# Kernel optimization log

Measured on AMD Instinct MI355X. Metric: run time of the kernel, lower is better.

Reference implementation:

```python
import jax, jax.numpy as jnp
import numpy as np

OBS, ACT, H = 64, 16, 64
T, B = 512, 4096


def _orth(key, shape):
    # orthogonal init like nn.init.orthogonal_ (gain 1 for predict; capture uses
    # gain sqrt(2) via init_ wrapper, but predict re-inits to plain orthogonal).
    a = jax.random.normal(key, shape, dtype=jnp.float32)
    q, r = jnp.linalg.qr(a if shape[0] >= shape[1] else a.T)
    q = q * jnp.sign(jnp.diag(r))
    return q if shape[0] >= shape[1] else q.T


def setup_inputs() -> dict:
    key = jax.random.key(0)
    ks = jax.random.split(key, 10)
    g2 = np.sqrt(2.0).astype(np.float32)
    inp = {
        "x": jax.random.normal(ks[0], (T, B, OBS), dtype=jnp.float32),
        "h": jax.random.normal(ks[1], (1, B, H), dtype=jnp.float32),
        "g": jax.random.uniform(ks[2], (T, B, 1), dtype=jnp.float32),
        "a": jax.random.normal(ks[3], (T, B, ACT), dtype=jnp.float32),
        # capture MLP: Linear(obs->H), tanh, Linear(H->H), tanh  (gain sqrt(2))
        "Wc1": g2 * _orth(ks[4], (OBS, H)),
        "bc1": jnp.zeros((H,), jnp.float32),
        "Wc2": g2 * _orth(ks[5], (H, H)),
        "bc2": jnp.zeros((H,), jnp.float32),
        # predict (Dynamics): Linear(H+ACT->H), tanh, Linear(H->H), tanh (gain 1)
        "Wp1": _orth(ks[6], (H + ACT, H)),
        "bp1": jnp.zeros((H,), jnp.float32),
        "Wp2": _orth(ks[7], (H, H)),
        "bp2": jnp.zeros((H,), jnp.float32),
    }
    return inp


def reference(x, h, g, a, Wc1, bc1, Wc2, bc2, Wp1, bp1, Wp2, bp2):
    # capture branch has no recurrent dependence -> compute for all t at once
    z1_all = jnp.tanh(jnp.tanh(x @ Wc1 + bc1) @ Wc2 + bc2)  # [T, B, H]

    def step(h_prev, inp):  # h_prev: [B, H]
        z1_t, g_t, a_t = inp
        ha = jnp.concatenate([h_prev, a_t], axis=-1)  # [B, H+ACT]
        z2 = jnp.tanh(jnp.tanh(ha @ Wp1 + bp1) @ Wp2 + bp2)
        h_new = (1.0 - g_t) * z1_t + g_t * z2
        return h_new, h_new

    h_final, outs = jax.lax.scan(step, h[0], (z1_all, g, a))
    capt = z1_all.reshape(-1, z1_all.shape[-1])  # torch.cat over [B,H] chunks -> [T*B, H]
    return outs, h_final[None], capt
```

## Files before the change

kernel.cpp:

```cpp
#include <hip/hip_runtime.h>
#include <hip/hip_bf16.h>

#define T_STEPS 512
#define BATCH   4096
#define ACT     16
#define HDIM    64
#define HA_S    168
#define T1_S    168
#define Z1_S    66

typedef short s8v __attribute__((ext_vector_type(8)));
typedef float f4v __attribute__((ext_vector_type(4)));

#define MFMA16(A, B, C) __builtin_amdgcn_mfma_f32_16x16x32_bf16((A), (B), (C), 0, 0, 0)

__device__ __forceinline__ unsigned pkbf(float a, float b) {
    unsigned r;
    asm("v_cvt_pk_bf16_f32 %0, %1, %2" : "=v"(r) : "v"(a), "v"(b));
    return r;
}
__device__ __forceinline__ float lo16f(unsigned p) { return __builtin_bit_cast(float, p << 16); }
__device__ __forceinline__ float hi16f(unsigned p) { return __builtin_bit_cast(float, p & 0xFFFF0000u); }

__device__ __forceinline__ unsigned short f2bf(float f) {
    unsigned u = __builtin_bit_cast(unsigned, f);
    u += 0x7FFFu + ((u >> 16) & 1u);
    return (unsigned short)(u >> 16);
}
__device__ __forceinline__ float bf2f(unsigned short b) {
    return __builtin_bit_cast(float, ((unsigned)b) << 16);
}

__device__ __forceinline__ float ftanh(float x) {
    float e = __expf(2.0f * x);
    return 1.0f - 2.0f * __builtin_amdgcn_rcpf(e + 1.0f);
}

#define BAR() do { \
    asm volatile("s_waitcnt lgkmcnt(0)" ::: "memory"); \
    __builtin_amdgcn_s_barrier(); \
    asm volatile("" ::: "memory"); \
} while (0)

__device__ __forceinline__ void stage_x(short* xsb, int row, int col, float4 v) {
    unsigned h0 = pkbf(v.x, v.y), h1 = pkbf(v.z, v.w);
    float r0 = v.x - lo16f(h0), r1 = v.y - hi16f(h0);
    float r2 = v.z - lo16f(h1), r3 = v.w - hi16f(h1);
    unsigned l0 = pkbf(r0, r1), l1 = pkbf(r2, r3);
    uint2 hh; hh.x = h0; hh.y = h1;
    uint2 ll; ll.x = l0; ll.y = l1;
    *reinterpret_cast<uint2*>(&xsb[row * T1_S + col])      = hh;
    *reinterpret_cast<uint2*>(&xsb[row * T1_S + 64 + col]) = ll;
}

__device__ __forceinline__ void cap_l1(const short* xsb, short* t1cb, int c, int kb, int rg, int n,
                                       s8v Wh0, s8v Wh1, s8v Wl0, s8v Wl1, float bias) {
    const short* xr_ = xsb + c * T1_S;
    s8v x0 = *(const s8v*)(xr_ + kb);
    s8v x1 = *(const s8v*)(xr_ + 32 + kb);
    s8v x2 = *(const s8v*)(xr_ + 64 + kb);
    s8v x3 = *(const s8v*)(xr_ + 96 + kb);
    f4v u0 = {bias, bias, bias, bias};
    f4v u1 = {0.f, 0.f, 0.f, 0.f}, u2 = u1, u3 = u1;
    u0 = MFMA16(x0, Wh0, u0); u1 = MFMA16(x1, Wh1, u1);
    u2 = MFMA16(x2, Wh0, u2); u3 = MFMA16(x3, Wh1, u3);
    u0 = MFMA16(x0, Wl0, u0); u1 = MFMA16(x1, Wl1, u1);
    #pragma unroll
    for (int r = 0; r < 4; ++r) {
        float tv = ftanh((u0[r] + u1[r]) + (u2[r] + u3[r]));
        unsigned ph = pkbf(tv, tv);
        float rr = tv - lo16f(ph);
        unsigned pl = pkbf(rr, rr);
        t1cb[(rg + r) * T1_S + n]      = (short)(ph & 0xFFFFu);
        t1cb[(rg + r) * T1_S + 64 + n] = (short)(pl & 0xFFFFu);
    }
}

__device__ __forceinline__ f4v cap_l2(const short* t1cb, int c, int kb,
                                      s8v Wh0, s8v Wh1, s8v Wl0, s8v Wl1, float bias) {
    const short* tr_ = t1cb + c * T1_S;
    s8v q0 = *(const s8v*)(tr_ + kb);
    s8v q1 = *(const s8v*)(tr_ + 32 + kb);
    s8v q2 = *(const s8v*)(tr_ + 64 + kb);
    s8v q3 = *(const s8v*)(tr_ + 96 + kb);
    f4v d0 = {bias, bias, bias, bias};
    f4v d1 = {0.f, 0.f, 0.f, 0.f}, d2 = d1, d3 = d1;
    d0 = MFMA16(q0, Wh0, d0); d1 = MFMA16(q1, Wh1, d1);
    d2 = MFMA16(q2, Wh0, d2); d3 = MFMA16(q3, Wh1, d3);
    d0 = MFMA16(q0, Wl0, d0); d1 = MFMA16(q1, Wl1, d1);
    f4v out;
    #pragma unroll
    for (int r = 0; r < 4; ++r)
        out[r] = ftanh((d0[r] + d1[r]) + (d2[r] + d3[r]));
    return out;
}

__global__ __launch_bounds__(512, 2) void fused_cell(
    const float* __restrict__ x,  const float* __restrict__ h0,
    const float* __restrict__ g,  const float* __restrict__ a,
    const float* __restrict__ Wc1, const float* __restrict__ bc1,
    const float* __restrict__ Wc2, const float* __restrict__ bc2,
    const float* __restrict__ Wp1, const float* __restrict__ bp1,
    const float* __restrict__ Wp2, const float* __restrict__ bp2,
    float* __restrict__ outs, float* __restrict__ hfin, float* __restrict__ capt)
{
    __shared__ short ha [16 * HA_S];
    __shared__ short t1s[16 * T1_S];
    __shared__ short t1c[16 * T1_S];
    __shared__ short xs [16 * T1_S];
    __shared__ float z1b[2][16 * Z1_S];

    const int tid = threadIdx.x;
    const int wv  = tid >> 6;
    const bool cap = wv >= 4;
    const int w   = wv & 3;
    const int l   = tid & 63;
    const int c   = l & 15;
    const int q   = l >> 4;
    const int n   = (w << 4) | c;
    const int rg  = q << 2;
    const int kb  = q << 3;
    const int b0  = blockIdx.x << 4;
    const int i2  = tid & 255;
    const int xrow = i2 >> 4;
    const int xcol = (i2 & 15) << 2;
    const int acol = i2 & 15;

    s8v F1h0, F1h1, F1l0, F1l1, Fa0, Fa1, F2h0, F2h1, F2l0, F2l1;
    {
        const float* W1 = cap ? Wc1 : Wp1;
        const float* W2 = cap ? Wc2 : Wp2;
        #pragma unroll
        for (int i = 0; i < 8; ++i) {
            const int k0 = kb + i, k1 = 32 + kb + i;
            float v; unsigned short h;
            v = W1[k0 * 64 + n]; h = f2bf(v); F1h0[i] = (short)h; F1l0[i] = (short)f2bf(v - bf2f(h));
            v = W1[k1 * 64 + n]; h = f2bf(v); F1h1[i] = (short)h; F1l1[i] = (short)f2bf(v - bf2f(h));
            v = W2[k0 * 64 + n]; h = f2bf(v); F2h0[i] = (short)h; F2l0[i] = (short)f2bf(v - bf2f(h));
            v = W2[k1 * 64 + n]; h = f2bf(v); F2h1[i] = (short)h; F2l1[i] = (short)f2bf(v - bf2f(h));
        }
        if (!cap) {
            #pragma unroll
            for (int i = 0; i < 8; ++i) {
                const int ca_ = 64 + ((kb + i) & 15);
                float v = Wp1[ca_ * 64 + n]; unsigned short h = f2bf(v);
                Fa0[i] = (short)h; Fa1[i] = (short)f2bf(v - bf2f(h));
            }
        }
    }
    const float bzA = cap ? bc1[n] : bp1[n];
    const float bzB = cap ? bc2[n] : bp2[n];

    #pragma unroll
    for (int j = 0; j < 2; ++j) {
        int id = tid + j * 512;
        int row = id >> 6, cc = id & 63;
        float v = h0[(b0 + row) * 64 + cc];
        unsigned ph = pkbf(v, v);
        float rr = v - lo16f(ph);
        unsigned pl = pkbf(rr, rr);
        ha[row * HA_S + cc]      = (short)(ph & 0xFFFFu);
        ha[row * HA_S + 64 + cc] = (short)(pl & 0xFFFFu);
    }
    if (cap) {
        float v = a[(long)(b0 + xrow) * ACT + acol];
        unsigned ph = pkbf(v, v);
        float rr = v - lo16f(ph);
        unsigned pl = pkbf(rr, rr);
        ha[xrow * HA_S + 128 + acol] = (short)(ph & 0xFFFFu);
        ha[xrow * HA_S + 144 + acol] = (short)(pl & 0xFFFFu);
    }
    float4 xp0;
    if (cap) xp0 = *(const float4*)&x[(long)(b0 + xrow) * 64 + xcol];
    __syncthreads();

    if (cap) stage_x(xs, xrow, xcol, xp0);
    __syncthreads();
    if (cap) cap_l1(xs, t1c, c, kb, rg, n, F1h0, F1h1, F1l0, F1l1, bzA);
    __syncthreads();

    float4 XC, XN;
    float  aC = 0.f, aN = 0.f;
    float  gC[4], gN[4];
    float  hl[4] = {0.f, 0.f, 0.f, 0.f};
    if (cap) {
        f4v z1o = cap_l2(t1c, c, kb, F2h0, F2h1, F2l0, F2l1, bzB);
        #pragma unroll
        for (int r = 0; r < 4; ++r) {
            z1b[0][(rg + r) * Z1_S + n] = z1o[r];
            capt[(long)(b0 + rg + r) * 64 + n] = z1o[r];
        }
        float4 x1v = *(const float4*)&x[((long)1 * BATCH + b0 + xrow) * 64 + xcol];
        stage_x(xs, xrow, xcol, x1v);
        XC = *(const float4*)&x[((long)2 * BATCH + b0 + xrow) * 64 + xcol];
        aC = a[((long)1 * BATCH + b0 + xrow) * ACT + acol];
    } else {
        #pragma unroll
        for (int r = 0; r < 4; ++r) gC[r] = g[b0 + rg + r];
        __builtin_amdgcn_s_setprio(1);
    }
    __syncthreads();

#define STEP(tt, PAR, GCv, GNv, ACv, ANv, XCv, XNv) {                           \
    const int t_  = (tt);                                                       \
    const int tp1 = (t_ + 1 < T_STEPS) ? t_ + 1 : T_STEPS - 1;                  \
    const int tp2 = (t_ + 2 < T_STEPS) ? t_ + 2 : T_STEPS - 1;                  \
    const int tp3 = (t_ + 3 < T_STEPS) ? t_ + 3 : T_STEPS - 1;                  \
                                 \
    if (!cap) {                                                                 \
        _Pragma("unroll")                                                       \
        for (int r = 0; r < 4; ++r)                                             \
            GNv[r] = g[(long)tp1 * BATCH + b0 + rg + r];                        \
        const short* har = &ha[c * HA_S];                                       \
        s8v af0 = *(const s8v*)(har + kb);                                      \
        s8v af1 = *(const s8v*)(har + 32 + kb);                                 \
        s8v af2 = *(const s8v*)(har + 64 + kb);                                 \
        s8v af3 = *(const s8v*)(har + 96 + kb);                                 \
        s8v afa = *(const s8v*)(har + 128 + kb);                                \
        f4v p0 = {bzA, bzA, bzA, bzA};                                          \
        f4v p1 = {0.f, 0.f, 0.f, 0.f}, p2 = p1, p3 = p1;                        \
        p0 = MFMA16(af0, F1h0, p0); p1 = MFMA16(af1, F1h1, p1);                 \
        p2 = MFMA16(af2, F1h0, p2); p3 = MFMA16(af3, F1h1, p3);                 \
        p0 = MFMA16(af0, F1l0, p0); p1 = MFMA16(af1, F1l1, p1);                 \
        p2 = MFMA16(afa, Fa0,  p2); p3 = MFMA16(afa, Fa1,  p3);                 \
        _Pragma("unroll")                                                       \
        for (int r = 0; r < 4; ++r) {                                           \
            float tv = ftanh((p0[r] + p1[r]) + (p2[r] + p3[r]));                \
            unsigned ph = pkbf(tv, tv);                                         \
            float rr = tv - lo16f(ph);                                          \
            unsigned pl = pkbf(rr, rr);                                         \
            t1s[(rg + r) * T1_S + n]      = (short)(ph & 0xFFFFu);              \
            t1s[(rg + r) * T1_S + 64 + n] = (short)(pl & 0xFFFFu);              \
        }                                                                       \
    } else {                                                                    \
        XNv = *(const float4*)&x[((long)tp3 * BATCH + b0 + xrow) * 64 + xcol];  \
        ANv = a[((long)tp2 * BATCH + b0 + xrow) * ACT + acol];                  \
        cap_l1(xs, t1c, c, kb, rg, n, F1h0, F1h1, F1l0, F1l1, bzA);             \
    }                                                                           \
    BAR();                                                                      \
                                 \
    if (!cap) {                                                                 \
        const short* t1r = &t1s[c * T1_S];                                      \
        s8v bq0 = *(const s8v*)(t1r + kb);                                      \
        s8v bq1 = *(const s8v*)(t1r + 32 + kb);                                 \
        s8v bq2 = *(const s8v*)(t1r + 64 + kb);                                 \
        s8v bq3 = *(const s8v*)(t1r + 96 + kb);                                 \
        f4v c0 = {bzB, bzB, bzB, bzB};                                          \
        f4v c1 = {0.f, 0.f, 0.f, 0.f}, c2 = c1, c3 = c1;                        \
        c0 = MFMA16(bq0, F2h0, c0); c1 = MFMA16(bq1, F2h1, c1);                 \
        c2 = MFMA16(bq2, F2h0, c2); c3 = MFMA16(bq3, F2h1, c3);                 \
        c0 = MFMA16(bq0, F2l0, c0); c1 = MFMA16(bq1, F2l1, c1);                 \
        _Pragma("unroll")                                                       \
        for (int r = 0; r < 4; ++r) {                                           \
            float z1v = z1b[PAR][(rg + r) * Z1_S + n];                          \
            float z2  = ftanh((c0[r] + c1[r]) + (c2[r] + c3[r]));               \
            float hv  = fmaf(GCv[r], z2 - z1v, z1v);                            \
            hl[r] = hv;                                                         \
            outs[((long)t_ * BATCH + b0 + rg + r) * 64 + n] = hv;               \
            unsigned ph = pkbf(hv, hv);                                         \
            float rr = hv - lo16f(ph);                                          \
            unsigned pl = pkbf(rr, rr);                                         \
            ha[(rg + r) * HA_S + n]      = (short)(ph & 0xFFFFu);               \
            ha[(rg + r) * HA_S + 64 + n] = (short)(pl & 0xFFFFu);               \
        }                                                                       \
    } else {                                                                    \
        f4v z1o = cap_l2(t1c, c, kb, F2h0, F2h1, F2l0, F2l1, bzB);              \
        _Pragma("unroll")                                                       \
        for (int r = 0; r < 4; ++r) {                                           \
            z1b[PAR ^ 1][(rg + r) * Z1_S + n] = z1o[r];                         \
            if (t_ < T_STEPS - 1)                                               \
                capt[((long)(t_ + 1) * BATCH + b0 + rg + r) * 64 + n] = z1o[r]; \
        }                                                                       \
        stage_x(xs, xrow, xcol, XCv);                         \
        {                                                                       \
            unsigned ph = pkbf(ACv, ACv);                   \
            float rr = ACv - lo16f(ph);                                         \
            unsigned pl = pkbf(rr, rr);                                         \
            ha[xrow * HA_S + 128 + acol] = (short)(ph & 0xFFFFu);               \
            ha[xrow * HA_S + 144 + acol] = (short)(pl & 0xFFFFu);               \
        }                                                                       \
    }                                                                           \
    BAR();                                                                      \
}

    for (int t = 0; t < T_STEPS; t += 2) {
        STEP(t,     0, gC, gN, aC, aN, XC, XN);
        STEP(t + 1, 1, gN, gC, aN, aC, XN, XC);
    }
#undef STEP

    if (!cap) {
        #pragma unroll
        for (int r = 0; r < 4; ++r)
            hfin[(long)(b0 + rg + r) * 64 + n] = hl[r];
    }
}

extern "C" void kernel_launch(void* const* d_in, const int* in_sizes, int n_in,
                              void* d_out, int out_size, void* d_ws, size_t ws_size,
                              hipStream_t stream) {
    const float* x   = (const float*)d_in[0];
    const float* h0  = (const float*)d_in[1];
    const float* g   = (const float*)d_in[2];
    const float* a   = (const float*)d_in[3];
    const float* Wc1 = (const float*)d_in[4];
    const float* bc1 = (const float*)d_in[5];
    const float* Wc2 = (const float*)d_in[6];
    const float* bc2 = (const float*)d_in[7];
    const float* Wp1 = (const float*)d_in[8];
    const float* bp1 = (const float*)d_in[9];
    const float* Wp2 = (const float*)d_in[10];
    const float* bp2 = (const float*)d_in[11];

    float* outs = (float*)d_out;
    float* hfin = outs + (long)T_STEPS * BATCH * HDIM;
    float* capt = hfin + (long)BATCH * HDIM;

    fused_cell<<<BATCH / 16, 512, 0, stream>>>(
        x, h0, g, a, Wc1, bc1, Wc2, bc2, Wp1, bp1, Wp2, bp2, outs, hfin, capt);
}
```

Before: 591.3 us.

## Drop low-order bf16 split terms from layer-1 and hidden-activation MFMAs

Removes the bf16 low-residual correction on first-layer weights, on the action weights and on the intermediate tanh activations. This cuts the first-layer MFMA count from 8 to 5 (predict) and 6 to 4 (capture), and the second-layer count from 6 to 4. The intermediate LDS buffers shrink to a single bf16 copy. The hidden-state and x splits are kept, and the code also adds precomputed LDS/global pointers, float4 gate loads and an fma-based tanh. Precision drops, so results may drift over 512 recurrent steps.

```diff
diff --git a/kernel.cpp b/kernel.cpp
--- a/kernel.cpp
+++ b/kernel.cpp
@@ -6,7 +6,8 @@
 #define ACT     16
 #define HDIM    64
 #define HA_S    168
-#define T1_S    168
+#define T1S_S   72
+#define XS_S    136
 #define Z1_S    66
 
 typedef short s8v __attribute__((ext_vector_type(8)));
@@ -33,7 +34,7 @@
 
 __device__ __forceinline__ float ftanh(float x) {
     float e = __expf(2.0f * x);
-    return 1.0f - 2.0f * __builtin_amdgcn_rcpf(e + 1.0f);
+    return fmaf(-2.0f, __builtin_amdgcn_rcpf(e + 1.0f), 1.0f);
 }
 
 #define BAR() do { \
@@ -42,57 +43,14 @@
     asm volatile("" ::: "memory"); \
 } while (0)
 
-__device__ __forceinline__ void stage_x(short* xsb, int row, int col, float4 v) {
-    unsigned h0 = pkbf(v.x, v.y), h1 = pkbf(v.z, v.w);
-    float r0 = v.x - lo16f(h0), r1 = v.y - hi16f(h0);
-    float r2 = v.z - lo16f(h1), r3 = v.w - hi16f(h1);
-    unsigned l0 = pkbf(r0, r1), l1 = pkbf(r2, r3);
-    uint2 hh; hh.x = h0; hh.y = h1;
-    uint2 ll; ll.x = l0; ll.y = l1;
-    *reinterpret_cast<uint2*>(&xsb[row * T1_S + col])      = hh;
-    *reinterpret_cast<uint2*>(&xsb[row * T1_S + 64 + col]) = ll;
-}
-
-__device__ __forceinline__ void cap_l1(const short* xsb, short* t1cb, int c, int kb, int rg, int n,
-                                       s8v Wh0, s8v Wh1, s8v Wl0, s8v Wl1, float bias) {
-    const short* xr_ = xsb + c * T1_S;
-    s8v x0 = *(const s8v*)(xr_ + kb);
-    s8v x1 = *(const s8v*)(xr_ + 32 + kb);
-    s8v x2 = *(const s8v*)(xr_ + 64 + kb);
-    s8v x3 = *(const s8v*)(xr_ + 96 + kb);
-    f4v u0 = {bias, bias, bias, bias};
-    f4v u1 = {0.f, 0.f, 0.f, 0.f}, u2 = u1, u3 = u1;
-    u0 = MFMA16(x0, Wh0, u0); u1 = MFMA16(x1, Wh1, u1);
-    u2 = MFMA16(x2, Wh0, u2); u3 = MFMA16(x3, Wh1, u3);
-    u0 = MFMA16(x0, Wl0, u0); u1 = MFMA16(x1, Wl1, u1);
-    #pragma unroll
-    for (int r = 0; r < 4; ++r) {
-        float tv = ftanh((u0[r] + u1[r]) + (u2[r] + u3[r]));
-        unsigned ph = pkbf(tv, tv);
-        float rr = tv - lo16f(ph);
-        unsigned pl = pkbf(rr, rr);
-        t1cb[(rg + r) * T1_S + n]      = (short)(ph & 0xFFFFu);
-        t1cb[(rg + r) * T1_S + 64 + n] = (short)(pl & 0xFFFFu);
-    }
-}
-
-__device__ __forceinline__ f4v cap_l2(const short* t1cb, int c, int kb,
-                                      s8v Wh0, s8v Wh1, s8v Wl0, s8v Wl1, float bias) {
-    const short* tr_ = t1cb + c * T1_S;
-    s8v q0 = *(const s8v*)(tr_ + kb);
-    s8v q1 = *(const s8v*)(tr_ + 32 + kb);
-    s8v q2 = *(const s8v*)(tr_ + 64 + kb);
-    s8v q3 = *(const s8v*)(tr_ + 96 + kb);
-    f4v d0 = {bias, bias, bias, bias};
-    f4v d1 = {0.f, 0.f, 0.f, 0.f}, d2 = d1, d3 = d1;
-    d0 = MFMA16(q0, Wh0, d0); d1 = MFMA16(q1, Wh1, d1);
-    d2 = MFMA16(q2, Wh0, d2); d3 = MFMA16(q3, Wh1, d3);
-    d0 = MFMA16(q0, Wl0, d0); d1 = MFMA16(q1, Wl1, d1);
-    f4v out;
-    #pragma unroll
-    for (int r = 0; r < 4; ++r)
-        out[r] = ftanh((d0[r] + d1[r]) + (d2[r] + d3[r]));
-    return out;
+__device__ __forceinline__ void stage_x(short* p, float4 v) {
+    unsigned h0p = pkbf(v.x, v.y), h1p = pkbf(v.z, v.w);
+    float r0 = v.x - lo16f(h0p), r1 = v.y - hi16f(h0p);
+    float r2 = v.z - lo16f(h1p), r3 = v.w - hi16f(h1p);
+    uint2 hh; hh.x = h0p; hh.y = h1p;
+    uint2 ll; ll.x = pkbf(r0, r1); ll.y = pkbf(r2, r3);
+    *reinterpret_cast<uint2*>(p)      = hh;
+    *reinterpret_cast<uint2*>(p + 64) = ll;
 }
 
 __global__ __launch_bounds__(512, 2) void fused_cell(
@@ -105,15 +63,14 @@
     float* __restrict__ outs, float* __restrict__ hfin, float* __restrict__ capt)
 {
     __shared__ short ha [16 * HA_S];
-    __shared__ short t1s[16 * T1_S];
-    __shared__ short t1c[16 * T1_S];
-    __shared__ short xs [16 * T1_S];
+    __shared__ short t1s[16 * T1S_S];
+    __shared__ short t1c[16 * T1S_S];
+    __shared__ short xs [16 * XS_S];
     __shared__ float z1b[2][16 * Z1_S];
 
     const int tid = threadIdx.x;
-    const int wv  = tid >> 6;
-    const bool cap = wv >= 4;
-    const int w   = wv & 3;
+    const bool cap = tid >= 256;
+    const int w   = (tid >> 6) & 3;
     const int l   = tid & 63;
     const int c   = l & 15;
     const int q   = l >> 4;
@@ -126,30 +83,42 @@
     const int xcol = (i2 & 15) << 2;
     const int acol = i2 & 15;
 
-    s8v F1h0, F1h1, F1l0, F1l1, Fa0, Fa1, F2h0, F2h1, F2l0, F2l1;
+    s8v F1h0, F1h1, Fa0, F2h0, F2h1, F2l0, F2l1;
     {
         const float* W1 = cap ? Wc1 : Wp1;
         const float* W2 = cap ? Wc2 : Wp2;
         #pragma unroll
         for (int i = 0; i < 8; ++i) {
             const int k0 = kb + i, k1 = 32 + kb + i;
-            float v; unsigned short h;
-            v = W1[k0 * 64 + n]; h = f2bf(v); F1h0[i] = (short)h; F1l0[i] = (short)f2bf(v - bf2f(h));
-            v = W1[k1 * 64 + n]; h = f2bf(v); F1h1[i] = (short)h; F1l1[i] = (short)f2bf(v - bf2f(h));
-            v = W2[k0 * 64 + n]; h = f2bf(v); F2h0[i] = (short)h; F2l0[i] = (short)f2bf(v - bf2f(h));
-            v = W2[k1 * 64 + n]; h = f2bf(v); F2h1[i] = (short)h; F2l1[i] = (short)f2bf(v - bf2f(h));
+            F1h0[i] = (short)f2bf(W1[k0 * 64 + n]);
+            F1h1[i] = (short)f2bf(W1[k1 * 64 + n]);
+            float v2a = W2[k0 * 64 + n]; unsigned short h2a = f2bf(v2a);
+            F2h0[i] = (short)h2a; F2l0[i] = (short)f2bf(v2a - bf2f(h2a));
+            float v2b = W2[k1 * 64 + n]; unsigned short h2b = f2bf(v2b);
+            F2h1[i] = (short)h2b; F2l1[i] = (short)f2bf(v2b - bf2f(h2b));
         }
         if (!cap) {
             #pragma unroll
-            for (int i = 0; i < 8; ++i) {
-                const int ca_ = 64 + ((kb + i) & 15);
-                float v = Wp1[ca_ * 64 + n]; unsigned short h = f2bf(v);
-                Fa0[i] = (short)h; Fa1[i] = (short)f2bf(v - bf2f(h));
-            }
+            for (int i = 0; i < 8; ++i)
+                Fa0[i] = (short)f2bf(Wp1[(64 + ((kb + i) & 15)) * 64 + n]);
         }
     }
-    const float bzA = cap ? bc1[n] : bp1[n];
-    const float bzB = cap ? bc2[n] : bp2[n];
+    const float bz1 = cap ? bc1[n] : bp1[n];
+    const float bz2 = cap ? bc2[n] : bp2[n];
+
+    const short* ha_rd  = &ha [c * HA_S];
+    short*       ha_wr  = &ha [rg * HA_S + n];
+    short*       ha_awr = &ha [xrow * HA_S + 128 + acol];
+    const short* t1s_rd = &t1s[c * T1S_S];
+    short*       t1s_wr = &t1s[rg * T1S_S + n];
+    const short* t1c_rd = &t1c[c * T1S_S];
+    short*       t1c_wr = &t1c[rg * T1S_S + n];
+    const short* xs_rd  = &xs [c * XS_S];
+    short*       xs_wr  = &xs [xrow * XS_S + xcol];
+    const float* z1r0 = &z1b[0][rg * Z1_S + n];
+    const float* z1r1 = &z1b[1][rg * Z1_S + n];
+    float*       z1w0 = &z1b[0][rg * Z1_S + n];
+    float*       z1w1 = &z1b[1][rg * Z1_S + n];
 
     #pragma unroll
     for (int j = 0; j < 2; ++j) {
@@ -158,134 +127,168 @@
         float v = h0[(b0 + row) * 64 + cc];
         unsigned ph = pkbf(v, v);
         float rr = v - lo16f(ph);
-        unsigned pl = pkbf(rr, rr);
-        ha[row * HA_S + cc]      = (short)(ph & 0xFFFFu);
-        ha[row * HA_S + 64 + cc] = (short)(pl & 0xFFFFu);
+        ha[row * HA_S + cc]      = (short)ph;
+        ha[row * HA_S + 64 + cc] = (short)pkbf(rr, rr);
     }
     if (cap) {
         float v = a[(long)(b0 + xrow) * ACT + acol];
         unsigned ph = pkbf(v, v);
         float rr = v - lo16f(ph);
-        unsigned pl = pkbf(rr, rr);
-        ha[xrow * HA_S + 128 + acol] = (short)(ph & 0xFFFFu);
-        ha[xrow * HA_S + 144 + acol] = (short)(pl & 0xFFFFu);
-    }
-    float4 xp0;
-    if (cap) xp0 = *(const float4*)&x[(long)(b0 + xrow) * 64 + xcol];
+        ha_awr[0]  = (short)ph;
+        ha_awr[16] = (short)pkbf(rr, rr);
+    }
     __syncthreads();
 
-    if (cap) stage_x(xs, xrow, xcol, xp0);
+    if (cap) {
+        float4 v0 = *(const float4*)&x[(long)(b0 + xrow) * 64 + xcol];
+        stage_x(xs_wr, v0);
+    }
     __syncthreads();
-    if (cap) cap_l1(xs, t1c, c, kb, rg, n, F1h0, F1h1, F1l0, F1l1, bzA);
+
+    if (cap) {
+        s8v x0 = *(const s8v*)(xs_rd + kb);
+        s8v x1 = *(const s8v*)(xs_rd + 32 + kb);
+        s8v x2 = *(const s8v*)(xs_rd + 64 + kb);
+        s8v x3 = *(const s8v*)(xs_rd + 96 + kb);
+        f4v p0 = {bz1, bz1, bz1, bz1};
+        f4v p1 = {0.f, 0.f, 0.f, 0.f}, p2 = p1, p3 = p1;
+        p0 = MFMA16(x0, F1h0, p0); p1 = MFMA16(x1, F1h1, p1);
+        p2 = MFMA16(x2, F1h0, p2); p3 = MFMA16(x3, F1h1, p3);
+        #pragma unroll
+        for (int r = 0; r < 4; ++r) {
+            float tv = ftanh((p0[r] + p1[r]) + (p2[r] + p3[r]));
+            t1c_wr[r * T1S_S] = (short)pkbf(tv, tv);
+        }
+    }
     __syncthreads();
 
     float4 XC, XN;
     float  aC = 0.f, aN = 0.f;
-    float  gC[4], gN[4];
+    float  gC4[4], gN4[4];
     float  hl[4] = {0.f, 0.f, 0.f, 0.f};
+    const float *gp = g, *xp = x, *ap = a;
+    float *outp = outs, *cp = capt;
+
     if (cap) {
-        f4v z1o = cap_l2(t1c, c, kb, F2h0, F2h1, F2l0, F2l1, bzB);
+        s8v q0_ = *(const s8v*)(t1c_rd + kb);
+        s8v q1_ = *(const s8v*)(t1c_rd + 32 + kb);
+        f4v d0 = {bz2, bz2, bz2, bz2};
+        f4v d1 = {0.f, 0.f, 0.f, 0.f};
+        d0 = MFMA16(q0_, F2h0, d0); d1 = MFMA16(q1_, F2h1, d1);
+        d0 = MFMA16(q0_, F2l0, d0); d1 = MFMA16(q1_, F2l1, d1);
         #pragma unroll
         for (int r = 0; r < 4; ++r) {
-            z1b[0][(rg + r) * Z1_S + n] = z1o[r];
-            capt[(long)(b0 + rg + r) * 64 + n] = z1o[r];
+            float zv = ftanh(d0[r] + d1[r]);
+            z1w0[r * Z1_S] = zv;
+            capt[(long)(b0 + rg + r) * 64 + n] = zv;
         }
-        float4 x1v = *(const float4*)&x[((long)1 * BATCH + b0 + xrow) * 64 + xcol];
-        stage_x(xs, xrow, xcol, x1v);
+        float4 x1v = *(const float4*)&x[((long)BATCH + b0 + xrow) * 64 + xcol];
+        stage_x(xs_wr, x1v);
         XC = *(const float4*)&x[((long)2 * BATCH + b0 + xrow) * 64 + xcol];
-        aC = a[((long)1 * BATCH + b0 + xrow) * ACT + acol];
+        aC = a[((long)BATCH + b0 + xrow) * ACT + acol];
+        xp = &x[((long)3 * BATCH + b0 + xrow) * 64 + xcol];
+        ap = &a[((long)2 * BATCH + b0 + xrow) * ACT + acol];
+        cp = &capt[((long)BATCH + b0 + rg) * 64 + n];
     } else {
         #pragma unroll
-        for (int r = 0; r < 4; ++r) gC[r] = g[b0 + rg + r];
+        for (int r = 0; r < 4; ++r) gC4[r] = g[b0 + rg + r];
+        gp   = &g[(long)BATCH + b0 + rg];
+        outp = &outs[(long)(b0 + rg) * 64 + n];
         __builtin_amdgcn_s_setprio(1);
     }
     __syncthreads();
 
-#define STEP(tt, PAR, GCv, GNv, ACv, ANv, XCv, XNv) {                           \
-    const int t_  = (tt);                                                       \
-    const int tp1 = (t_ + 1 < T_STEPS) ? t_ + 1 : T_STEPS - 1;                  \
-    const int tp2 = (t_ + 2 < T_STEPS) ? t_ + 2 : T_STEPS - 1;                  \
-    const int tp3 = (t_ + 3 < T_STEPS) ? t_ + 3 : T_STEPS - 1;                  \
-                                 \
-    if (!cap) {                                                                 \
-        _Pragma("unroll")                                                       \
-        for (int r = 0; r < 4; ++r)                                             \
-            GNv[r] = g[(long)tp1 * BATCH + b0 + rg + r];                        \
-        const short* har = &ha[c * HA_S];                                       \
-        s8v af0 = *(const s8v*)(har + kb);                                      \
-        s8v af1 = *(const s8v*)(har + 32 + kb);                                 \
-        s8v af2 = *(const s8v*)(har + 64 + kb);                                 \
-        s8v af3 = *(const s8v*)(har + 96 + kb);                                 \
-        s8v afa = *(const s8v*)(har + 128 + kb);                                \
-        f4v p0 = {bzA, bzA, bzA, bzA};                                          \
-        f4v p1 = {0.f, 0.f, 0.f, 0.f}, p2 = p1, p3 = p1;                        \
-        p0 = MFMA16(af0, F1h0, p0); p1 = MFMA16(af1, F1h1, p1);                 \
-        p2 = MFMA16(af2, F1h0, p2); p3 = MFMA16(af3, F1h1, p3);                 \
-        p0 = MFMA16(af0, F1l0, p0); p1 = MFMA16(af1, F1l1, p1);                 \
-        p2 = MFMA16(afa, Fa0,  p2); p3 = MFMA16(afa, Fa1,  p3);                 \
-        _Pragma("unroll")                                                       \
-        for (int r = 0; r < 4; ++r) {                                           \
-            float tv = ftanh((p0[r] + p1[r]) + (p2[r] + p3[r]));                \
-            unsigned ph = pkbf(tv, tv);                                         \
-            float rr = tv - lo16f(ph);                                          \
-            unsigned pl = pkbf(rr, rr);                                         \
-            t1s[(rg + r) * T1_S + n]      = (short)(ph & 0xFFFFu);              \
-            t1s[(rg + r) * T1_S + 64 + n] = (short)(pl & 0xFFFFu);              \
-        }                                                                       \
-    } else {                                                                    \
-        XNv = *(const float4*)&x[((long)tp3 * BATCH + b0 + xrow) * 64 + xcol];  \
-        ANv = a[((long)tp2 * BATCH + b0 + xrow) * ACT + acol];                  \
-        cap_l1(xs, t1c, c, kb, rg, n, F1h0, F1h1, F1l0, F1l1, bzA);             \
-    }                                                                           \
-    BAR();                                                                      \
-                                 \
-    if (!cap) {                                                                 \
-        const short* t1r = &t1s[c * T1_S];                                      \
-        s8v bq0 = *(const s8v*)(t1r + kb);                                      \
-        s8v bq1 = *(const s8v*)(t1r + 32 + kb);                                 \
-        s8v bq2 = *(const s8v*)(t1r + 64 + kb);                                 \
-        s8v bq3 = *(const s8v*)(t1r + 96 + kb);                                 \
-        f4v c0 = {bzB, bzB, bzB, bzB};                                          \
-        f4v c1 = {0.f, 0.f, 0.f, 0.f}, c2 = c1, c3 = c1;                        \
-        c0 = MFMA16(bq0, F2h0, c0); c1 = MFMA16(bq1, F2h1, c1);                 \
-        c2 = MFMA16(bq2, F2h0, c2); c3 = MFMA16(bq3, F2h1, c3);                 \
-        c0 = MFMA16(bq0, F2l0, c0); c1 = MFMA16(bq1, F2l1, c1);                 \
-        _Pragma("unroll")                                                       \
-        for (int r = 0; r < 4; ++r) {                                           \
-            float z1v = z1b[PAR][(rg + r) * Z1_S + n];                          \
-            float z2  = ftanh((c0[r] + c1[r]) + (c2[r] + c3[r]));               \
-            float hv  = fmaf(GCv[r], z2 - z1v, z1v);                            \
-            hl[r] = hv;                                                         \
-            outs[((long)t_ * BATCH + b0 + rg + r) * 64 + n] = hv;               \
-            unsigned ph = pkbf(hv, hv);                                         \
-            float rr = hv - lo16f(ph);                                          \
-            unsigned pl = pkbf(rr, rr);                                         \
-            ha[(rg + r) * HA_S + n]      = (short)(ph & 0xFFFFu);               \
-            ha[(rg + r) * HA_S + 64 + n] = (short)(pl & 0xFFFFu);               \
-        }                                                                       \
-    } else {                                                                    \
-        f4v z1o = cap_l2(t1c, c, kb, F2h0, F2h1, F2l0, F2l1, bzB);              \
-        _Pragma("unroll")                                                       \
-        for (int r = 0; r < 4; ++r) {                                           \
-            z1b[PAR ^ 1][(rg + r) * Z1_S + n] = z1o[r];                         \
-            if (t_ < T_STEPS - 1)                                               \
-                capt[((long)(t_ + 1) * BATCH + b0 + rg + r) * 64 + n] = z1o[r]; \
-        }                                                                       \
-        stage_x(xs, xrow, xcol, XCv);                         \
-        {                                                                       \
-            unsigned ph = pkbf(ACv, ACv);                   \
-            float rr = ACv - lo16f(ph);                                         \
-            unsigned pl = pkbf(rr, rr);                                         \
-            ha[xrow * HA_S + 128 + acol] = (short)(ph & 0xFFFFu);               \
-            ha[xrow * HA_S + 144 + acol] = (short)(pl & 0xFFFFu);               \
-        }                                                                       \
-    }                                                                           \
-    BAR();                                                                      \
+#define STEP(tt, PAR, GCv, GNv, ACv, ANv, XCv, XNv) {                         \
+    const int t_ = (tt);                                                      \
+                               \
+    if (!cap) {                                                               \
+        float4 gv = *(const float4*)gp;                                       \
+        GNv[0] = gv.x; GNv[1] = gv.y; GNv[2] = gv.z; GNv[3] = gv.w;           \
+        if (t_ + 2 < T_STEPS) gp += BATCH;                                    \
+        s8v af0 = *(const s8v*)(ha_rd + kb);                                  \
+        s8v af1 = *(const s8v*)(ha_rd + 32 + kb);                             \
+        s8v af2 = *(const s8v*)(ha_rd + 64 + kb);                             \
+        s8v af3 = *(const s8v*)(ha_rd + 96 + kb);                             \
+        s8v afa = *(const s8v*)(ha_rd + 128 + kb);                            \
+        f4v p0 = {bz1, bz1, bz1, bz1};                                        \
+        f4v p1 = {0.f, 0.f, 0.f, 0.f}, p2 = p1, p3 = p1;                      \
+        p0 = MFMA16(af0, F1h0, p0); p1 = MFMA16(af1, F1h1, p1);               \
+        p2 = MFMA16(af2, F1h0, p2); p3 = MFMA16(af3, F1h1, p3);               \
+        p2 = MFMA16(afa, Fa0,  p2);                                           \
+        _Pragma("unroll")                                                     \
+        for (int r = 0; r < 4; ++r) {                                         \
+            float tv = ftanh((p0[r] + p1[r]) + (p2[r] + p3[r]));              \
+            t1s_wr[r * T1S_S] = (short)pkbf(tv, tv);                          \
+        }                                                                     \
+    } else {                                                                  \
+        XNv = *(const float4*)xp;                                             \
+        if (t_ + 4 < T_STEPS) xp += (long)BATCH * 64;                         \
+        ANv = *ap;                                                            \
+        if (t_ + 3 < T_STEPS) ap += BATCH * ACT;                              \
+        s8v x0 = *(const s8v*)(xs_rd + kb);                                   \
+        s8v x1 = *(const s8v*)(xs_rd + 32 + kb);                              \
+        s8v x2 = *(const s8v*)(xs_rd + 64 + kb);                              \
+        s8v x3 = *(const s8v*)(xs_rd + 96 + kb);                              \
+        f4v p0 = {bz1, bz1, bz1, bz1};                                        \
+        f4v p1 = {0.f, 0.f, 0.f, 0.f}, p2 = p1, p3 = p1;                      \
+        p0 = MFMA16(x0, F1h0, p0); p1 = MFMA16(x1, F1h1, p1);                 \
+        p2 = MFMA16(x2, F1h0, p2); p3 = MFMA16(x3, F1h1, p3);                 \
+        _Pragma("unroll")                                                     \
+        for (int r = 0; r < 4; ++r) {                                         \
+            float tv = ftanh((p0[r] + p1[r]) + (p2[r] + p3[r]));              \
+            t1c_wr[r * T1S_S] = (short)pkbf(tv, tv);                          \
+        }                                                                     \
+    }                                                                         \
+    BAR();                                                                    \
+                               \
+    if (!cap) {                                                               \
+        s8v bq0 = *(const s8v*)(t1s_rd + kb);                                 \
+        s8v bq1 = *(const s8v*)(t1s_rd + 32 + kb);                            \
+        f4v c0 = {bz2, bz2, bz2, bz2};                                        \
+        f4v c1 = {0.f, 0.f, 0.f, 0.f};                                        \
+        c0 = MFMA16(bq0, F2h0, c0); c1 = MFMA16(bq1, F2h1, c1);               \
+        c0 = MFMA16(bq0, F2l0, c0); c1 = MFMA16(bq1, F2l1, c1);               \
+        const float* zr = (PAR) ? z1r1 : z1r0;                                \
+        _Pragma("unroll")                                                     \
+        for (int r = 0; r < 4; ++r) {                                         \
+            float z1v = zr[r * Z1_S];                                         \
+            float z2  = ftanh(c0[r] + c1[r]);                                 \
+            float hv  = fmaf(GCv[r], z2 - z1v, z1v);                          \
+            hl[r] = hv;                                                       \
+            outp[r * HDIM] = hv;                                              \
+            unsigned ph = pkbf(hv, hv);                                       \
+            float rr = hv - lo16f(ph);                                        \
+            ha_wr[r * HA_S]      = (short)ph;                                 \
+            ha_wr[r * HA_S + 64] = (short)pkbf(rr, rr);                       \
+        }                                                                     \
+        outp += (long)BATCH * HDIM;                                           \
+    } else {                                                                  \
+        s8v q0_ = *(const s8v*)(t1c_rd + kb);                                 \
+        s8v q1_ = *(const s8v*)(t1c_rd + 32 + kb);                            \
+        f4v d0 = {bz2, bz2, bz2, bz2};                                        \
+        f4v d1 = {0.f, 0.f, 0.f, 0.f};                                        \
+        d0 = MFMA16(q0_, F2h0, d0); d1 = MFMA16(q1_, F2h1, d1);               \
+        d0 = MFMA16(q0_, F2l0, d0); d1 = MFMA16(q1_, F2l1, d1);               \
+        float* zw = (PAR) ? z1w0 : z1w1;                                      \
+        _Pragma("unroll")                                                     \
+        for (int r = 0; r < 4; ++r) {                                         \
+            float zv = ftanh(d0[r] + d1[r]);                                  \
+            zw[r * Z1_S] = zv;                                                \
+            if (t_ < T_STEPS - 1) cp[r * HDIM] = zv;                          \
+        }                                                                     \
+        cp += (long)BATCH * HDIM;                                             \
+        stage_x(xs_wr, XCv);                                \
+        unsigned ph = pkbf(ACv, ACv);                     \
+        float rr = ACv - lo16f(ph);                                           \
+        ha_awr[0]  = (short)ph;                                               \
+        ha_awr[16] = (short)pkbf(rr, rr);                                     \
+    }                                                                         \
+    BAR();                                                                    \
 }
 
     for (int t = 0; t < T_STEPS; t += 2) {
-        STEP(t,     0, gC, gN, aC, aN, XC, XN);
-        STEP(t + 1, 1, gN, gC, aN, aC, XN, XC);
+        STEP(t,     0, gC4, gN4, aC, aN, XC, XN);
+        STEP(t + 1, 1, gN4, gC4, aN, aC, XN, XC);
     }
 #undef STEP
 
```

After: 581.2 us. Within noise of the previous version (-1.7%).
